# Kernel optimization log

Measured on AMD Instinct MI355X. Metric: run time of the kernel, lower is better.

The kernel has to match this reference:

```python
import jax, jax.numpy as jnp
import numpy as np

B, T, C = 8, 2048, 1024
HS = 128           # head_size
N_TERMS = 2
THETA = 10000.0


def _rope_tables(dim, end):
    freqs = 1.0 / (THETA ** (jnp.arange(0, dim, 2, dtype=jnp.float32) / dim))  # [dim/2]
    ang = jnp.arange(end, dtype=jnp.float32)[:, None] * freqs[None, :]          # [end, dim/2]
    return jnp.cos(ang), jnp.sin(ang)


def _apply_rope(x, cos, sin):
    # x: [..., T, D]; pairs are interleaved (x0,x1),(x2,x3),...
    xr = x[..., 0::2]
    xi = x[..., 1::2]
    or_ = xr * cos - xi * sin
    oi = xr * sin + xi * cos
    return jnp.stack([or_, oi], axis=-1).reshape(x.shape)


def setup_inputs() -> dict:
    key = jax.random.key(0)
    ks = jax.random.split(key, 6)
    x = jax.random.normal(ks[0], (B, T, C), dtype=jnp.float32)
    Wq = jax.random.normal(ks[1], (N_TERMS, C, HS), dtype=jnp.float32) * 0.02
    Wk = jax.random.normal(ks[2], (N_TERMS, C, HS), dtype=jnp.float32) * 0.02
    Wv = jax.random.normal(ks[3], (C, 2 * HS), dtype=jnp.float32) * 0.02
    lambda_q = jax.random.normal(ks[4], (N_TERMS, HS), dtype=jnp.float32) * 0.1
    lambda_k = jax.random.normal(ks[5], (N_TERMS, HS), dtype=jnp.float32) * 0.1
    return {"x": x, "Wq": Wq, "Wk": Wk, "Wv": Wv,
            "lambda_q": lambda_q, "lambda_k": lambda_k, "layer_idx": 3}


def reference(x, Wq, Wk, Wv, lambda_q, lambda_k, layer_idx):
    Bx, Tx, Cx = x.shape
    n = Wq.shape[0]
    scale = 1.0 / (HS ** 0.5)

    v = x @ Wv                                   # [B,T,2*HS]
    q = jnp.einsum('btc,ncd->nbtd', x, Wq)       # [n,B,T,HS]
    k = jnp.einsum('btc,ncd->nbtd', x, Wk)

    cos, sin = _rope_tables(HS, Tx)              # [T, HS/2]
    q = _apply_rope(q, cos, sin)
    k = _apply_rope(k, cos, sin)

    att = jnp.einsum('nbtd,nbsd->nbts', q, k) * scale  # [n,B,T,T]
    causal = jnp.tril(jnp.ones((Tx, Tx), dtype=bool))
    att = jnp.where(causal, att, -jnp.inf)
    att = jax.nn.softmax(att, axis=-1)

    # lambda values
    lam_init = 0.8 - 0.6 * jnp.exp(-0.3 * (jnp.float32(layer_idx) - 1.0))
    e = jnp.mean(jnp.exp(lambda_q * lambda_k), axis=-1)         # [n]
    e_prev = jnp.concatenate([jnp.zeros((1,), e.dtype), e[:-1]])
    lam = e - e_prev + lam_init                                 # [n]
    signs = jnp.where(jnp.arange(n) % 2 == 1, -1.0, 1.0)

    diff_att = jnp.einsum('n,nbts->bts', signs * lam, att)      # [B,T,T]
    out = diff_att @ v                                          # [B,T,2*HS]
    return out
```

## Files before the change

### kernel.cpp

```cpp
#include <hip/hip_runtime.h>
#include <math.h>

#define B_DIM 8
#define T_DIM 2048
#define C_DIM 1024
#define HS_DIM 128
#define VD 256
#define M_DIM (B_DIM * T_DIM)
#define QK_ELEMS (M_DIM * HS_DIM)
#define SCALE 0.088388347648318447f
#define LOG_THETA 9.210340371976184f

#define QB_OFF   0u
#define KB_OFF   4194304u
#define VT_OFF   8388608u
#define WT_OFF   12582912u
#define XBH_OFF  13369344u
#define LAM_OFF  21757952u
#define XSPLIT_ELEMS 8388608u

typedef short s8v   __attribute__((ext_vector_type(8)));
typedef float f32x4 __attribute__((ext_vector_type(4)));
typedef float f32x16 __attribute__((ext_vector_type(16)));

__device__ __forceinline__ unsigned int bf16_rne(float f) {
    unsigned int u = __float_as_uint(f);
    return (u + 0x7fffu + ((u >> 16) & 1u)) >> 16;
}
__device__ __forceinline__ unsigned int pack_bf2(float lo, float hi) {
    return bf16_rne(lo) | (bf16_rne(hi) << 16);
}
__device__ __forceinline__ void async_cp16(const unsigned short* g, unsigned short* l) {
    __builtin_amdgcn_global_load_lds(
        (const __attribute__((address_space(1))) unsigned int*)g,
        (__attribute__((address_space(3))) unsigned int*)l, 16, 0, 0);
}

__global__ void lam_kernel(const float* __restrict__ lq, const float* __restrict__ lk,
                           const int* __restrict__ lidx, float* __restrict__ lam_out) {
    int t = threadIdx.x;
    float s0 = expf(lq[t] * lk[t]) + expf(lq[t + 64] * lk[t + 64]);
    float s1 = expf(lq[128 + t] * lk[128 + t]) + expf(lq[192 + t] * lk[192 + t]);
    #pragma unroll
    for (int off = 32; off > 0; off >>= 1) {
        s0 += __shfl_down(s0, off);
        s1 += __shfl_down(s1, off);
    }
    if (t == 0) {
        float e0 = s0 * (1.0f / 128.0f);
        float e1 = s1 * (1.0f / 128.0f);
        float li = 0.8f - 0.6f * expf(-0.3f * ((float)lidx[0] - 1.0f));
        lam_out[0] = e0 + li;
        lam_out[1] = -(e1 - e0 + li);
    }
}

__global__ __launch_bounds__(256) void cast_x_kernel(const float* __restrict__ x,
                                                     unsigned short* __restrict__ lo,
                                                     unsigned short* __restrict__ hi) {
    const size_t i8 = ((size_t)blockIdx.x * 256 + threadIdx.x) * 8;
    float4 a = *(const float4*)(x + i8);
    float4 b = *(const float4*)(x + i8 + 4);
    uint4 u;
    u.x = pack_bf2(a.x, a.y); u.y = pack_bf2(a.z, a.w);
    u.z = pack_bf2(b.x, b.y); u.w = pack_bf2(b.z, b.w);
    unsigned short* dst = (i8 < XSPLIT_ELEMS) ? (lo + i8) : (hi + (i8 - XSPLIT_ELEMS));
    *(uint4*)dst = u;
}

__global__ __launch_bounds__(256) void cast_wt_kernel(
    const float* __restrict__ Wq, const float* __restrict__ Wk,
    const float* __restrict__ Wv, unsigned short* __restrict__ wt) {
    __shared__ float tile[32][33];
    const int t = threadIdx.x;
    const int n0 = blockIdx.x * 32;
    const int k0 = blockIdx.y * 32;
    const int seg = n0 >> 7;
    const int nl = t & 31;
    const int ng = n0 + nl;
    const int ngl = ng & 127;
    const int pcol = 2 * ((ngl & 15) + ((ngl >> 5) << 4)) + ((ngl >> 4) & 1);
    const float* src; int ld;
    if (seg < 2)      { src = Wq + (size_t)seg * (C_DIM * HS_DIM) + pcol; ld = 128; }
    else if (seg < 4) { src = Wk + (size_t)(seg - 2) * (C_DIM * HS_DIM) + pcol; ld = 128; }
    else              { src = Wv + (ng - 512); ld = 256; }
    #pragma unroll
    for (int rep = 0; rep < 4; ++rep) {
        int kl = (t >> 5) + rep * 8;
        tile[kl][nl] = src[(size_t)(k0 + kl) * ld];
    }
    __syncthreads();
    unsigned int* wt32 = (unsigned int*)wt;
    #pragma unroll
    for (int rep = 0; rep < 2; ++rep) {
        int nl2 = (t >> 4) + rep * 16;
        int k2 = (t & 15) * 2;
        unsigned int u = pack_bf2(tile[k2][nl2], tile[k2 + 1][nl2]);
        wt32[((size_t)(n0 + nl2) * 1024 + k0 + k2) >> 1] = u;
    }
}

__global__ __launch_bounds__(256) void gemm_kernel(
    const unsigned short* __restrict__ xlo, const unsigned short* __restrict__ xhi,
    const unsigned short* __restrict__ wt,
    unsigned short* __restrict__ qo, unsigned short* __restrict__ ko,
    unsigned short* __restrict__ vo) {
    __shared__ unsigned short As[128 * 32];
    __shared__ unsigned short Bs[128 * 32];

    const int t = threadIdx.x;
    const int wv = t >> 6, lane = t & 63;
    const int quad = lane >> 4, l15 = lane & 15;
    const int m0 = blockIdx.x * 128;
    const int n0 = blockIdx.y * 128;
    const int wr = wv >> 1, wc = wv & 1;

    const unsigned short* xbase = (m0 < 8192)
        ? (xlo + (size_t)m0 * C_DIM) : (xhi + (size_t)(m0 - 8192) * C_DIM);

    f32x4 acc[4][4];
    #pragma unroll
    for (int i = 0; i < 4; ++i)
        #pragma unroll
        for (int j = 0; j < 4; ++j) acc[i][j] = (f32x4){0.f, 0.f, 0.f, 0.f};

    const int srow = lane >> 2;
    const int skof = (lane & 3) * 8;

    for (int k0 = 0; k0 < C_DIM; k0 += 32) {
        #pragma unroll
        for (int j = 0; j < 2; ++j) {
            const int c = wv * 2 + j;
            async_cp16(xbase + (size_t)(c * 16 + srow) * C_DIM + k0 + skof, As + c * 512);
        }
        #pragma unroll
        for (int j = 0; j < 2; ++j) {
            const int c = wv * 2 + j;
            async_cp16(wt + (size_t)(n0 + c * 16 + srow) * C_DIM + k0 + skof, Bs + c * 512);
        }
        __syncthreads();
        s8v af[4], bf[4];
        #pragma unroll
        for (int i = 0; i < 4; ++i)
            af[i] = *(const s8v*)&As[(wr * 64 + i * 16 + l15) * 32 + quad * 8];
        #pragma unroll
        for (int j = 0; j < 4; ++j)
            bf[j] = *(const s8v*)&Bs[(wc * 64 + j * 16 + l15) * 32 + quad * 8];
        #pragma unroll
        for (int i = 0; i < 4; ++i)
            #pragma unroll
            for (int j = 0; j < 4; ++j)
                acc[i][j] = __builtin_amdgcn_mfma_f32_16x16x32_bf16(af[i], bf[j], acc[i][j], 0, 0, 0);
        __syncthreads();
    }

    const int seg = n0 >> 7;
    if (seg < 4) {
        unsigned short* dstbuf = ((seg < 2) ? qo : ko) + (size_t)(seg & 1) * QK_ELEMS;
        const int mi0 = l15 + 32 * wc;
        const int mi1 = mi0 + 16;
        const float freq0 = __expf((float)mi0 * (-LOG_THETA / 64.f));
        const float freq1 = __expf((float)mi1 * (-LOG_THETA / 64.f));
        #pragma unroll
        for (int i = 0; i < 4; ++i) {
            #pragma unroll
            for (int e = 0; e < 4; ++e) {
                const int m = m0 + wr * 64 + i * 16 + quad * 4 + e;
                const float trow = (float)(m & (T_DIM - 1));
                unsigned int* p32 = (unsigned int*)(dstbuf + (size_t)m * HS_DIM);
                float sn0, cs0, sn1, cs1;
                __sincosf(trow * freq0, &sn0, &cs0);
                __sincosf(trow * freq1, &sn1, &cs1);
                const float xr0 = acc[i][0][e], xi0 = acc[i][1][e];
                const float xr1 = acc[i][2][e], xi1 = acc[i][3][e];
                p32[mi0] = pack_bf2(xr0 * cs0 - xi0 * sn0, xr0 * sn0 + xi0 * cs0);
                p32[mi1] = pack_bf2(xr1 * cs1 - xi1 * sn1, xr1 * sn1 + xi1 * cs1);
            }
        }
    } else {
        const int bq = m0 >> 11;
        const int tbase = m0 & (T_DIM - 1);
        unsigned int* vT32 = (unsigned int*)vo;
        #pragma unroll
        for (int j = 0; j < 4; ++j) {
            const int d = (seg - 4) * 128 + wc * 64 + j * 16 + l15;
            const size_t rowbase = (size_t)(bq * VD + d) * (T_DIM / 2);
            #pragma unroll
            for (int i = 0; i < 4; ++i) {
                const int tok = tbase + wr * 64 + i * 16 + quad * 4;
                uint2 u;
                u.x = pack_bf2(acc[i][j][0], acc[i][j][1]);
                u.y = pack_bf2(acc[i][j][2], acc[i][j][3]);
                *(uint2*)&vT32[rowbase + (tok >> 1)] = u;
            }
        }
    }
}

#define KSTR 136
#define VSTR 72
#define PSTR 72
#define OSTR 260
#define K_OFF 0
#define V_OFF 34816
#define P_OFF 71680
#define PSZ  9216
#define SM_TOTAL 90112

__global__ __launch_bounds__(512, 1) void attn_kernel(
    const unsigned short* __restrict__ qg, const unsigned short* __restrict__ kg,
    const unsigned short* __restrict__ vg, const float* __restrict__ lam,
    float* __restrict__ outp) {
    __shared__ __align__(16) unsigned char smem[SM_TOTAL];
    unsigned short* Ks = (unsigned short*)(smem + K_OFF);
    unsigned short* Vt = (unsigned short*)(smem + V_OFF);

    const int t = threadIdx.x;
    const int id = blockIdx.x;
    const int b = id & 7;
    const int kp = id >> 3;

    const int w = t >> 6, lane = t & 63;
    const int l31 = lane & 31, lh = lane >> 5;
    const int sg = w >> 2;
    const int term = w & 1;
    const int kh = (w >> 1) & 1;

    const int strip = sg ? kp : (63 - kp);
    const int q0 = strip * 32;
    const int ntS = (strip >> 1) + 1;
    const int ntB = ((63 - kp) >> 1) + 1;

    unsigned short* Ps = (unsigned short*)(smem + P_OFF + sg * PSZ);
    float* Lsum = (float*)(smem + P_OFF + sg * PSZ);
    float* Ol = (float*)(smem + sg * V_OFF);

    const float cn = lam[term];

    const unsigned short* qrow = qg
        + ((size_t)(term * B_DIM + b) * T_DIM + q0 + l31) * HS_DIM + lh * 8;
    s8v qa[8];
    #pragma unroll
    for (int ks = 0; ks < 8; ++ks)
        qa[ks] = *(const s8v*)(qrow + ks * 16);

    f32x16 o[4];
    #pragma unroll
    for (int dt = 0; dt < 4; ++dt)
        #pragma unroll
        for (int r = 0; r < 16; ++r) o[dt][r] = 0.f;
    float l_acc[16];
    #pragma unroll
    for (int r = 0; r < 16; ++r) l_acc[r] = 0.f;

    for (int it = 0; it < ntB; ++it) {
        const int s0 = it * 64;
        #pragma unroll
        for (int rep = 0; rep < 4; ++rep) {
            int idx = t + rep * 512;
            int n = idx >> 10, rem = idx & 1023;
            int r = rem >> 4, seg = rem & 15;
            const uint4 g = *(const uint4*)(kg
                + ((size_t)(n * B_DIM + b) * T_DIM + s0 + r) * HS_DIM + seg * 8);
            *(uint4*)&Ks[(n * 64 + r) * KSTR + seg * 8] = g;
        }
        #pragma unroll
        for (int rep = 0; rep < 4; ++rep) {
            int idx = t + rep * 512;
            int d = idx >> 3, seg = idx & 7;
            const uint4 g = *(const uint4*)(vg
                + ((size_t)(b * VD + d) * T_DIM + s0) + seg * 8);
            *(uint4*)&Vt[d * VSTR + seg * 8] = g;
        }
        __syncthreads();

        if (it < ntS) {
            f32x16 sc;
            #pragma unroll
            for (int r = 0; r < 16; ++r) sc[r] = 0.f;
            #pragma unroll
            for (int ks = 0; ks < 8; ++ks) {
                s8v kf = *(const s8v*)&Ks[(term * 64 + kh * 32 + l31) * KSTR
                                          + ks * 16 + lh * 8];
                sc = __builtin_amdgcn_mfma_f32_32x32x16_bf16(qa[ks], kf, sc, 0, 0, 0);
            }
            const int key = s0 + kh * 32 + l31;
            #pragma unroll
            for (int r = 0; r < 16; ++r) {
                const int row = (r & 3) + 8 * (r >> 2) + 4 * lh;
                const float p = (key <= q0 + row) ? __expf(sc[r] * SCALE) : 0.f;
                l_acc[r] += p;
                Ps[(term * 32 + row) * PSTR + kh * 32 + l31] = (unsigned short)bf16_rne(p);
            }
        }
        __syncthreads();

        if (it < ntS) {
            #pragma unroll
            for (int ks = 0; ks < 4; ++ks) {
                s8v pa = *(const s8v*)&Ps[(term * 32 + l31) * PSTR + ks * 16 + lh * 8];
                #pragma unroll
                for (int dt = 0; dt < 4; ++dt) {
                    s8v vb = *(const s8v*)&Vt[(kh * 128 + dt * 32 + l31) * VSTR
                                              + ks * 16 + lh * 8];
                    o[dt] = __builtin_amdgcn_mfma_f32_32x32x16_bf16(pa, vb, o[dt], 0, 0, 0);
                }
            }
        }
        __syncthreads();
    }

    #pragma unroll
    for (int r = 0; r < 16; ++r) {
        float lt = l_acc[r];
        #pragma unroll
        for (int off = 1; off < 32; off <<= 1) lt += __shfl_xor(lt, off);
        if (l31 == 0) {
            const int row = (r & 3) + 8 * (r >> 2) + 4 * lh;
            Lsum[(term * 2 + kh) * 32 + row] = lt;
        }
    }
    __syncthreads();
    float inv[16];
    #pragma unroll
    for (int r = 0; r < 16; ++r) {
        const int row = (r & 3) + 8 * (r >> 2) + 4 * lh;
        inv[r] = cn / (Lsum[(term * 2 + 0) * 32 + row] + Lsum[(term * 2 + 1) * 32 + row]);
    }

    if (term) {
        #pragma unroll
        for (int dt = 0; dt < 4; ++dt)
            #pragma unroll
            for (int r = 0; r < 16; ++r) {
                const int row = (r & 3) + 8 * (r >> 2) + 4 * lh;
                Ol[row * OSTR + kh * 128 + dt * 32 + l31] = o[dt][r] * inv[r];
            }
    }
    __syncthreads();
    if (!term) {
        #pragma unroll
        for (int dt = 0; dt < 4; ++dt)
            #pragma unroll
            for (int r = 0; r < 16; ++r) {
                const int row = (r & 3) + 8 * (r >> 2) + 4 * lh;
                Ol[row * OSTR + kh * 128 + dt * 32 + l31] += o[dt][r] * inv[r];
            }
    }
    __syncthreads();
    #pragma unroll
    for (int rep = 0; rep < 8; ++rep) {
        int idx = (t & 255) + rep * 256;
        int row = idx >> 6, c4 = idx & 63;
        float4 val = *(const float4*)&Ol[row * OSTR + c4 * 4];
        *(float4*)&outp[((size_t)(b * T_DIM + q0 + row)) * VD + c4 * 4] = val;
    }
}

extern "C" void kernel_launch(void* const* d_in, const int* in_sizes, int n_in,
                              void* d_out, int out_size, void* d_ws, size_t ws_size,
                              hipStream_t stream) {
    const float* x  = (const float*)d_in[0];
    const float* Wq = (const float*)d_in[1];
    const float* Wk = (const float*)d_in[2];
    const float* Wv = (const float*)d_in[3];
    const float* lq = (const float*)d_in[4];
    const float* lk = (const float*)d_in[5];
    const int* lidx = (const int*)d_in[6];

    unsigned short* ws = (unsigned short*)d_ws;
    unsigned short* qb   = ws + QB_OFF;
    unsigned short* kb   = ws + KB_OFF;
    unsigned short* vTb  = ws + VT_OFF;
    unsigned short* wtb  = ws + WT_OFF;
    unsigned short* xbhi = ws + XBH_OFF;
    float* lamb = (float*)(ws + LAM_OFF);
    unsigned short* xblo = (unsigned short*)d_out;
    (void)ws_size; (void)in_sizes; (void)n_in; (void)out_size;

    lam_kernel<<<dim3(1), dim3(64), 0, stream>>>(lq, lk, lidx, lamb);
    cast_x_kernel<<<dim3(8192), dim3(256), 0, stream>>>(x, xblo, xbhi);
    cast_wt_kernel<<<dim3(24, 32), dim3(256), 0, stream>>>(Wq, Wk, Wv, wtb);
    gemm_kernel<<<dim3(128, 6), dim3(256), 0, stream>>>(xblo, xbhi, wtb, qb, kb, vTb);
    attn_kernel<<<dim3(256), dim3(512), 0, stream>>>(qb, kb, vTb, lamb, (float*)d_out);
}
```

Measured before the change: 228.3 us.

## Double-buffer K/V tiles with async global-to-LDS copies and XOR swizzle

Replaces the synchronous per-iteration K/V loads into padded LDS with asynchronous 16-byte global-to-LDS copies into two alternating buffers, prefetching the next 64-key tile while the current one is computed. The padded strides are replaced by an XOR swizzle to avoid bank conflicts, and MFMA sections are wrapped in s_setprio. One barrier becomes a raw waitcnt+barrier. LDS use grows to about 146 KB, and correctness now depends on async_cp16 completing before the final per-iteration sync.

```diff
diff --git a/kernel.cpp b/kernel.cpp
--- a/kernel.cpp
+++ b/kernel.cpp
@@ -197,23 +197,18 @@
     }
 }
 
-#define KSTR 136
-#define VSTR 72
 #define PSTR 72
 #define OSTR 260
-#define K_OFF 0
-#define V_OFF 34816
-#define P_OFF 71680
+#define BUFB 65536
+#define P_OFF 131072
 #define PSZ  9216
-#define SM_TOTAL 90112
+#define SM_TOTAL 149504
 
 __global__ __launch_bounds__(512, 1) void attn_kernel(
     const unsigned short* __restrict__ qg, const unsigned short* __restrict__ kg,
     const unsigned short* __restrict__ vg, const float* __restrict__ lam,
     float* __restrict__ outp) {
     __shared__ __align__(16) unsigned char smem[SM_TOTAL];
-    unsigned short* Ks = (unsigned short*)(smem + K_OFF);
-    unsigned short* Vt = (unsigned short*)(smem + V_OFF);
 
     const int t = threadIdx.x;
     const int id = blockIdx.x;
@@ -233,7 +228,7 @@
 
     unsigned short* Ps = (unsigned short*)(smem + P_OFF + sg * PSZ);
     float* Lsum = (float*)(smem + P_OFF + sg * PSZ);
-    float* Ol = (float*)(smem + sg * V_OFF);
+    float* Ol = (float*)(smem + sg * BUFB);
 
     const float cn = lam[term];
 
@@ -244,6 +239,21 @@
     for (int ks = 0; ks < 8; ++ks)
         qa[ks] = *(const s8v*)(qrow + ks * 16);
 
+    unsigned int kOffA[4], vOffA[4];
+    #pragma unroll
+    for (int rep = 0; rep < 4; ++rep) {
+        const int c = t + rep * 512;
+        const int rowg = c >> 4, slot = c & 15;
+        const int kterm = rowg >> 6, krow = rowg & 63;
+        const int kss = slot ^ (krow & 15);
+        kOffA[rep] = (unsigned int)(((kterm * B_DIM + b) * T_DIM + krow) * HS_DIM
+                                    + kss * 8);
+        const int drow = rowg;
+        const int vss = slot ^ (drow & 15);
+        const int dim = 2 * drow + (vss >> 3), tokc = vss & 7;
+        vOffA[rep] = (unsigned int)((b * VD + dim) * T_DIM + tokc * 8);
+    }
+
     f32x16 o[4];
     #pragma unroll
     for (int dt = 0; dt < 4; ++dt)
@@ -253,37 +263,49 @@
     #pragma unroll
     for (int r = 0; r < 16; ++r) l_acc[r] = 0.f;
 
+    {
+        unsigned short* kb0 = (unsigned short*)(smem + w * 1024);
+        unsigned short* vb0 = (unsigned short*)(smem + 32768 + w * 1024);
+        #pragma unroll
+        for (int rep = 0; rep < 4; ++rep) {
+            async_cp16(kg + kOffA[rep], kb0 + rep * 4096);
+            async_cp16(vg + vOffA[rep], vb0 + rep * 4096);
+        }
+    }
+    __syncthreads();
+
+    const int krow = kh * 32 + l31;
+    const int k15 = l31 & 15;
+
     for (int it = 0; it < ntB; ++it) {
         const int s0 = it * 64;
-        #pragma unroll
-        for (int rep = 0; rep < 4; ++rep) {
-            int idx = t + rep * 512;
-            int n = idx >> 10, rem = idx & 1023;
-            int r = rem >> 4, seg = rem & 15;
-            const uint4 g = *(const uint4*)(kg
-                + ((size_t)(n * B_DIM + b) * T_DIM + s0 + r) * HS_DIM + seg * 8);
-            *(uint4*)&Ks[(n * 64 + r) * KSTR + seg * 8] = g;
-        }
-        #pragma unroll
-        for (int rep = 0; rep < 4; ++rep) {
-            int idx = t + rep * 512;
-            int d = idx >> 3, seg = idx & 7;
-            const uint4 g = *(const uint4*)(vg
-                + ((size_t)(b * VD + d) * T_DIM + s0) + seg * 8);
-            *(uint4*)&Vt[d * VSTR + seg * 8] = g;
-        }
-        __syncthreads();
+        const unsigned char* buf = smem + (it & 1) * BUFB;
+
+        if (it + 1 < ntB) {
+            const int sn = s0 + 64;
+            unsigned char* nbuf = smem + ((it + 1) & 1) * BUFB;
+            unsigned short* kbn = (unsigned short*)(nbuf + w * 1024);
+            unsigned short* vbn = (unsigned short*)(nbuf + 32768 + w * 1024);
+            #pragma unroll
+            for (int rep = 0; rep < 4; ++rep) {
+                async_cp16(kg + kOffA[rep] + (size_t)sn * HS_DIM, kbn + rep * 4096);
+                async_cp16(vg + vOffA[rep] + sn, vbn + rep * 4096);
+            }
+        }
 
         if (it < ntS) {
+            const unsigned short* Kb = (const unsigned short*)buf;
             f32x16 sc;
             #pragma unroll
             for (int r = 0; r < 16; ++r) sc[r] = 0.f;
+            __builtin_amdgcn_s_setprio(1);
             #pragma unroll
             for (int ks = 0; ks < 8; ++ks) {
-                s8v kf = *(const s8v*)&Ks[(term * 64 + kh * 32 + l31) * KSTR
-                                          + ks * 16 + lh * 8];
+                const int x = (ks * 2 + lh) ^ k15;
+                s8v kf = *(const s8v*)&Kb[(term * 64 + krow) * 128 + x * 8];
                 sc = __builtin_amdgcn_mfma_f32_32x32x16_bf16(qa[ks], kf, sc, 0, 0, 0);
             }
+            __builtin_amdgcn_s_setprio(0);
             const int key = s0 + kh * 32 + l31;
             #pragma unroll
             for (int r = 0; r < 16; ++r) {
@@ -293,19 +315,25 @@
                 Ps[(term * 32 + row) * PSTR + kh * 32 + l31] = (unsigned short)bf16_rne(p);
             }
         }
-        __syncthreads();
+        asm volatile("s_waitcnt lgkmcnt(0)\n\ts_barrier" ::: "memory");
+        __builtin_amdgcn_sched_barrier(0);
 
         if (it < ntS) {
+            const unsigned short* Vb = (const unsigned short*)(buf + 32768);
+            __builtin_amdgcn_s_setprio(1);
             #pragma unroll
             for (int ks = 0; ks < 4; ++ks) {
                 s8v pa = *(const s8v*)&Ps[(term * 32 + l31) * PSTR + ks * 16 + lh * 8];
                 #pragma unroll
                 for (int dt = 0; dt < 4; ++dt) {
-                    s8v vb = *(const s8v*)&Vt[(kh * 128 + dt * 32 + l31) * VSTR
-                                              + ks * 16 + lh * 8];
+                    const int dim = kh * 128 + dt * 32 + l31;
+                    const int drow = dim >> 1;
+                    const int x = ((dim & 1) * 8 + ks * 2 + lh) ^ (drow & 15);
+                    s8v vb = *(const s8v*)&Vb[(drow * 16 + x) * 8];
                     o[dt] = __builtin_amdgcn_mfma_f32_32x32x16_bf16(pa, vb, o[dt], 0, 0, 0);
                 }
             }
+            __builtin_amdgcn_s_setprio(0);
         }
         __syncthreads();
     }
```

Result: faster. 213.7 us (-6.4%).
